# Optimization experiments

Measured on AMD Instinct MI355X. Metric: run time of the kernel, lower is better.

The kernel has to match this reference:

```python
import jax, jax.numpy as jnp
import numpy as np

B, N, C = 128, 36, 1024
K_NB = 16            # neighbors per node (top-k, includes loop)
KERNEL = 8           # number of Gaussian kernels
OUT = 1024           # out_dim; per-kernel out = OUT // KERNEL
PI = np.float32(np.pi)


def setup_inputs() -> dict:
    key = jax.random.key(0)
    ks = jax.random.split(key, 9)
    node_feats = jax.random.normal(ks[0], (B, N, C), dtype=jnp.float32)
    node_centre = jax.random.uniform(ks[1], (B, N, 2), dtype=jnp.float32)
    neighbor_idx = jax.random.randint(ks[2], (B * N, K_NB), 0, B * N, dtype=jnp.int32)
    graph_weights = jax.random.uniform(ks[3], (B * N * K_NB, 1), dtype=jnp.float32)
    # Gaussian kernel params (per reset_parameters)
    mean_rho = jax.random.uniform(ks[4], (1, KERNEL), dtype=jnp.float32)
    mean_theta = jax.random.uniform(ks[5], (1, KERNEL), minval=-PI, maxval=PI, dtype=jnp.float32)
    precision_rho = jax.random.uniform(ks[6], (1, KERNEL), minval=0.5, maxval=1.0, dtype=jnp.float32)
    precision_theta = jax.random.uniform(ks[7], (1, KERNEL), minval=0.5, maxval=1.0, dtype=jnp.float32)
    # per-kernel Linear(node_dim, out_dim//kernel, bias=False), stacked: [K, d_out_k, C]
    conv_w = jax.random.normal(ks[8], (KERNEL, OUT // KERNEL, C), dtype=jnp.float32) * (1.0 / np.sqrt(C))
    return {
        "node_feats": node_feats,
        "node_centre": node_centre,
        "neighbor_idx": neighbor_idx,
        "graph_weights": graph_weights,
        "mean_rho": mean_rho,
        "mean_theta": mean_theta,
        "precision_rho": precision_rho,
        "precision_theta": precision_theta,
        "conv_w": conv_w,
    }


def _forward(node_feats, node_centre, graph_weights,
             mean_rho, mean_theta, precision_rho, precision_theta,
             conv_w, neighbor_idx):
    b, n, c = node_feats.shape
    bn = b * n
    # pseudo polar coordinates per edge: centre_i - centre_j
    centre = node_centre.reshape(bn, 2)                       # [BN, 2]
    diff = centre[:, None, :] - centre[neighbor_idx]          # [BN, K_nb, 2]
    coord_x = diff[..., 0].reshape(-1)                        # [E]
    coord_y = diff[..., 1].reshape(-1)
    rho = jnp.sqrt(coord_x ** 2 + coord_y ** 2)
    theta = jnp.arctan2(coord_x, coord_y)
    # Gaussian mixture membership weights over KERNEL kernels
    w_rho = jnp.exp(-0.5 * (rho[:, None] - mean_rho) ** 2 / (1e-14 + precision_rho ** 2))
    first_angle = jnp.abs(theta[:, None] - mean_theta)
    second_angle = jnp.abs(2.0 * PI - first_angle)
    w_theta = jnp.exp(-0.5 * jnp.minimum(first_angle, second_angle) ** 2 / (1e-14 + precision_theta ** 2))
    weights = w_rho * w_theta                                  # [E, KERNEL]
    weights = jnp.where(jnp.isnan(weights), 0.0, weights)
    weights = weights / jnp.sum(weights, axis=1, keepdims=True)
    # combine with graph edge weights
    edge_w = graph_weights * weights                           # [E, KERNEL]
    edge_w = edge_w.reshape(bn, K_NB, KERNEL).transpose(0, 2, 1)  # [BN, K, K_nb]
    # gather neighbor features and weighted aggregate (bmm)
    nbr = node_feats.reshape(bn, c)[neighbor_idx]              # [BN, K_nb, C]
    agg = jnp.einsum('ekn,enc->ekc', edge_w, nbr)              # [BN, KERNEL, C]
    agg = agg.reshape(b, n, KERNEL, c)
    # per-kernel linear then concat over kernel dim
    out = jnp.einsum('bnkc,kdc->bnkd', agg, conv_w)            # [B, N, KERNEL, OUT//KERNEL]
    out = out.reshape(b, n, -1)                                # [B, N, OUT]
    return jax.nn.relu(out)


def reference(node_feats, node_centre, neighbor_idx, graph_weights,
              mean_rho, mean_theta, precision_rho, precision_theta, conv_w):
    return _forward(node_feats, node_centre, graph_weights,
                    mean_rho, mean_theta, precision_rho, precision_theta,
                    conv_w, neighbor_idx)
```

## Files before the change

kernel.cpp:

```cpp
#include <hip/hip_runtime.h>
#include <hip/hip_bf16.h>
#include <stdint.h>

#define B_DIM   128
#define N_DIM   36
#define C_DIM   1024
#define KNB     16
#define NKER    8
#define OUTD    1024
#define BN_NODES (B_DIM * N_DIM)
#define E_EDGES  (BN_NODES * KNB)
#define PI_F 3.14159265358979323846f

#define TM 64
#define TN 128
#define BK 64
#define KIT (C_DIM / BK)
#define CLP 136
#define A_OFF(p) ((p) * TM * BK)
#define B_OFF(p) (2 * TM * BK + (p) * TN * BK)

typedef __attribute__((ext_vector_type(8))) short bf16x8;
typedef __attribute__((ext_vector_type(4))) float floatx4;

struct alignas(8) U16x4 { unsigned short x, y, z, w; };

__device__ __forceinline__ unsigned short f2bf(float f) {
  union { float f; uint32_t u; } v; v.f = f;
  uint32_t u = v.u;
  return (unsigned short)((u + 0x7fffu + ((u >> 16) & 1u)) >> 16);
}
__device__ __forceinline__ float bf2f_lo(uint32_t pair) {
  union { uint32_t u; float f; } v; v.u = pair << 16;
  return v.f;
}
__device__ __forceinline__ float bf2f_hi(uint32_t pair) {
  union { uint32_t u; float f; } v; v.u = pair & 0xffff0000u;
  return v.f;
}

__device__ __forceinline__ void gload16(const void* g, void* l) {
  __builtin_amdgcn_global_load_lds((__attribute__((address_space(1))) void*)(g),
                                   (__attribute__((address_space(3))) void*)(l),
                                   16, 0, 0);
}

__global__ __launch_bounds__(256)
void cast_ew_kernel(const float* __restrict__ feats,
                    const float* __restrict__ cw,
                    const float* __restrict__ centre,
                    const int*   __restrict__ nbr,
                    const float* __restrict__ gw,
                    const float* __restrict__ mrho,
                    const float* __restrict__ mth,
                    const float* __restrict__ prho,
                    const float* __restrict__ pth,
                    unsigned short* __restrict__ fb,
                    unsigned short* __restrict__ wb,
                    float* __restrict__ ewg)
{
  const int NF4 = (BN_NODES * C_DIM) / 4;
  const int NW4 = (C_DIM * OUTD) / 4;
  int tid = blockIdx.x * 256 + threadIdx.x;
  if (tid < NF4) {
    float4 v = ((const float4*)feats)[tid];
    U16x4 o = { f2bf(v.x), f2bf(v.y), f2bf(v.z), f2bf(v.w) };
    ((U16x4*)fb)[tid] = o;
  } else {
    int t = tid - NF4;
    if (t < NW4) {
      float4 v = ((const float4*)cw)[t];
      U16x4 o = { f2bf(v.x), f2bf(v.y), f2bf(v.z), f2bf(v.w) };
      ((U16x4*)wb)[t] = o;
    } else {
      int e = t - NW4;
      if (e < E_EDGES) {
        int n = e >> 4;
        int m = nbr[e];
        float cx = centre[2 * n]     - centre[2 * m];
        float cy = centre[2 * n + 1] - centre[2 * m + 1];
        float rho   = sqrtf(cx * cx + cy * cy);
        float theta = atan2f(cx, cy);
        float wk[NKER];
        float s = 0.f;
#pragma unroll
        for (int k = 0; k < NKER; ++k) {
          float dr = rho - mrho[k];
          float pr = prho[k];
          float w_r = expf(-0.5f * dr * dr / (1e-14f + pr * pr));
          float fa = fabsf(theta - mth[k]);
          float sa = fabsf(2.0f * PI_F - fa);
          float mm = fminf(fa, sa);
          float pt = pth[k];
          float w_t = expf(-0.5f * mm * mm / (1e-14f + pt * pt));
          float ww = w_r * w_t;
          wk[k] = (ww != ww) ? 0.f : ww;
          s += wk[k];
        }
        float scale = gw[e] / s;
        int j = e & 15;
#pragma unroll
        for (int k = 0; k < NKER; ++k)
          ewg[(size_t)n * (NKER * KNB) + k * KNB + j] = wk[k] * scale;
      }
    }
  }
}

__global__ __launch_bounds__(256)
void gemm_bt(const unsigned short* __restrict__ A,
             const unsigned short* __restrict__ Bt,
             unsigned short* __restrict__ D)
{
  __shared__ unsigned short smem[2 * TM * BK + 2 * TN * BK];

  const int tid  = threadIdx.x;
  const int lane = tid & 63;
  const int wave = tid >> 6;
  const int wm   = wave >> 1;
  const int wn   = wave & 1;
  const int row0 = blockIdx.x * TM;
  const int col0 = blockIdx.y * TN;

  const int q  = lane >> 4;
  const int lr = lane & 15;

  floatx4 acc[2][4] = {};

  int offA[2], offB[4];
#pragma unroll
  for (int i = 0; i < 2; ++i) {
    int c = tid + 256 * i, row = c >> 3, qc = c & 7;
    offA[i] = (row0 + row) * C_DIM + (qc ^ (row & 7)) * 8;
  }
#pragma unroll
  for (int i = 0; i < 4; ++i) {
    int c = tid + 256 * i, row = c >> 3, qc = c & 7;
    offB[i] = (col0 + row) * C_DIM + (qc ^ (row & 7)) * 8;
  }

#define DMA(T, P) do {                                                       \
    _Pragma("unroll") for (int i = 0; i < 2; ++i)                            \
      gload16(A + offA[i] + (T) * BK,                                        \
              &smem[A_OFF(P) + (tid + 256 * i) * 8]);                        \
    _Pragma("unroll") for (int i = 0; i < 4; ++i)                            \
      gload16(Bt + offB[i] + (T) * BK,                                       \
              &smem[B_OFF(P) + (tid + 256 * i) * 8]);                        \
  } while (0)

  DMA(0, 0);

  for (int t = 0; t < KIT; ++t) {
    const int p = t & 1;
    __syncthreads();
    if (t + 1 < KIT) DMA(t + 1, 1 - p);

    const int aBase = A_OFF(p);
    const int bBase = B_OFF(p);
#pragma unroll
    for (int kc = 0; kc < 2; ++kc) {
      const int sc = ((kc * 4 + q) ^ (lr & 7)) * 8;
      bf16x8 af[2], bfr[4];
#pragma unroll
      for (int i = 0; i < 2; ++i)
        af[i]  = *(const bf16x8*)&smem[aBase + (wm * 32 + i * 16 + lr) * BK + sc];
#pragma unroll
      for (int j = 0; j < 4; ++j)
        bfr[j] = *(const bf16x8*)&smem[bBase + (wn * 64 + j * 16 + lr) * BK + sc];
#pragma unroll
      for (int i = 0; i < 2; ++i)
#pragma unroll
        for (int j = 0; j < 4; ++j)
          acc[i][j] = __builtin_amdgcn_mfma_f32_16x16x32_bf16(
              af[i], bfr[j], acc[i][j], 0, 0, 0);
    }
  }
#undef DMA

  __syncthreads();
#pragma unroll
  for (int i = 0; i < 2; ++i)
#pragma unroll
    for (int j = 0; j < 4; ++j)
#pragma unroll
      for (int r = 0; r < 4; ++r)
        smem[(wm * 32 + i * 16 + q * 4 + r) * CLP + wn * 64 + j * 16 + lr] =
            f2bf(acc[i][j][r]);
  __syncthreads();
#pragma unroll
  for (int i = 0; i < 4; ++i) {
    int c = tid + 256 * i;
    int row = c >> 4, qc = c & 15;
    *(uint4*)&D[(size_t)(row0 + row) * OUTD + col0 + qc * 8] =
        *(const uint4*)&smem[row * CLP + qc * 8];
  }
}

__global__ __launch_bounds__(256)
void agg_gather(const unsigned short* __restrict__ proj,
                const int*   __restrict__ nbr,
                const float* __restrict__ ewg,
                float* __restrict__ out)
{
  __shared__ int   idx[8][KNB];
  __shared__ float ewl[8][2][KNB];

  const int bid = blockIdx.x;
  const int x   = bid & 7;
  const int s   = x >> 1;
  const int g   = ((bid >> 3) << 1) | (x & 1);
  const int n0  = g * 8;
  const int t   = threadIdx.x;

  if (t < 128)
    idx[t >> 4][t & 15] = nbr[(n0 + (t >> 4)) * KNB + (t & 15)];
  {
    int a = t >> 5, r = t & 31;
    ewl[a][r >> 4][r & 15] = ewg[(size_t)(n0 + a) * (NKER * KNB) + s * 32 + r];
  }
  __syncthreads();

  const int a   = t >> 5;
  const int cu  = t & 31;
  const int kk  = cu >> 4;
  const int n   = n0 + a;
  const int ch0 = s * 256 + cu * 8;

  float acc[8] = {0.f, 0.f, 0.f, 0.f, 0.f, 0.f, 0.f, 0.f};
#pragma unroll
  for (int j = 0; j < KNB; ++j) {
    float wv = ewl[a][kk][j];
    uint4 v = *(const uint4*)&proj[(size_t)idx[a][j] * OUTD + ch0];
    acc[0] += wv * bf2f_lo(v.x);  acc[1] += wv * bf2f_hi(v.x);
    acc[2] += wv * bf2f_lo(v.y);  acc[3] += wv * bf2f_hi(v.y);
    acc[4] += wv * bf2f_lo(v.z);  acc[5] += wv * bf2f_hi(v.z);
    acc[6] += wv * bf2f_lo(v.w);  acc[7] += wv * bf2f_hi(v.w);
  }
  float4 r0, r1;
  r0.x = fmaxf(acc[0], 0.f); r0.y = fmaxf(acc[1], 0.f);
  r0.z = fmaxf(acc[2], 0.f); r0.w = fmaxf(acc[3], 0.f);
  r1.x = fmaxf(acc[4], 0.f); r1.y = fmaxf(acc[5], 0.f);
  r1.z = fmaxf(acc[6], 0.f); r1.w = fmaxf(acc[7], 0.f);
  float* o = out + (size_t)n * OUTD + ch0;
  *(float4*)(o)     = r0;
  *(float4*)(o + 4) = r1;
}

extern "C" void kernel_launch(void* const* d_in, const int* in_sizes, int n_in,
                              void* d_out, int out_size, void* d_ws, size_t ws_size,
                              hipStream_t stream)
{
  const float* feats  = (const float*)d_in[0];
  const float* centre = (const float*)d_in[1];
  const int*   nbr    = (const int*)  d_in[2];
  const float* gw     = (const float*)d_in[3];
  const float* mrho   = (const float*)d_in[4];
  const float* mth    = (const float*)d_in[5];
  const float* prho   = (const float*)d_in[6];
  const float* pth    = (const float*)d_in[7];
  const float* cw     = (const float*)d_in[8];
  float* out = (float*)d_out;

  char* ws = (char*)d_ws;
  unsigned short* fb   = (unsigned short*)(ws);
  unsigned short* wb   = (unsigned short*)(ws + 9437184);
  unsigned short* proj = (unsigned short*)(ws + 11534336);
  float*          ewg  = (float*)         (ws + 20971520);

  const int NF4 = (BN_NODES * C_DIM) / 4;
  const int NW4 = (C_DIM * OUTD) / 4;
  const int EWB = (E_EDGES + 255) / 256;
  cast_ew_kernel<<<dim3((NF4 + NW4) / 256 + EWB), dim3(256), 0, stream>>>(
      feats, cw, centre, nbr, gw, mrho, mth, prho, pth, fb, wb, ewg);
  gemm_bt<<<dim3(BN_NODES / TM, OUTD / TN), dim3(256), 0, stream>>>(fb, wb, proj);
  agg_gather<<<dim3(BN_NODES / 2), dim3(256), 0, stream>>>(proj, nbr, ewg, out);
}
```

Baseline: 122.3 us.

## Fuse fp32-to-bf16 feature cast into GEMM A-tile loads

Removes the separate pass that converts node features to bf16 in workspace. The GEMM now reads fp32 features straight from global memory into registers, converts them, and writes bf16 into shared memory. This saves one full read-write round trip of the feature matrix. The row tile shrinks from 64 to 48 and the wave layout changes to 1x4, so the grid divides evenly over 4608 rows. In exchange the A operand now uses register-staged loads instead of direct global-to-LDS DMA, and each block does less work.

```diff
diff --git a/kernel.cpp b/kernel.cpp
--- a/kernel.cpp
+++ b/kernel.cpp
@@ -12,7 +12,7 @@
 #define E_EDGES  (BN_NODES * KNB)
 #define PI_F 3.14159265358979323846f
 
-#define TM 64
+#define TM 48
 #define TN 128
 #define BK 64
 #define KIT (C_DIM / BK)
@@ -23,7 +23,8 @@
 typedef __attribute__((ext_vector_type(8))) short bf16x8;
 typedef __attribute__((ext_vector_type(4))) float floatx4;
 
-struct alignas(8) U16x4 { unsigned short x, y, z, w; };
+struct alignas(8)  U16x4 { unsigned short x, y, z, w; };
+struct alignas(16) U16x8 { unsigned short s[8]; };
 
 __device__ __forceinline__ unsigned short f2bf(float f) {
   union { float f; uint32_t u; } v; v.f = f;
@@ -46,149 +47,161 @@
 }
 
 __global__ __launch_bounds__(256)
-void cast_ew_kernel(const float* __restrict__ feats,
-                    const float* __restrict__ cw,
-                    const float* __restrict__ centre,
-                    const int*   __restrict__ nbr,
-                    const float* __restrict__ gw,
-                    const float* __restrict__ mrho,
-                    const float* __restrict__ mth,
-                    const float* __restrict__ prho,
-                    const float* __restrict__ pth,
-                    unsigned short* __restrict__ fb,
-                    unsigned short* __restrict__ wb,
-                    float* __restrict__ ewg)
-{
-  const int NF4 = (BN_NODES * C_DIM) / 4;
+void castw_ew_kernel(const float* __restrict__ cw,
+                     const float* __restrict__ centre,
+                     const int*   __restrict__ nbr,
+                     const float* __restrict__ gw,
+                     const float* __restrict__ mrho,
+                     const float* __restrict__ mth,
+                     const float* __restrict__ prho,
+                     const float* __restrict__ pth,
+                     unsigned short* __restrict__ wb,
+                     float* __restrict__ ewg)
+{
   const int NW4 = (C_DIM * OUTD) / 4;
   int tid = blockIdx.x * 256 + threadIdx.x;
-  if (tid < NF4) {
-    float4 v = ((const float4*)feats)[tid];
+  if (tid < NW4) {
+    float4 v = ((const float4*)cw)[tid];
     U16x4 o = { f2bf(v.x), f2bf(v.y), f2bf(v.z), f2bf(v.w) };
-    ((U16x4*)fb)[tid] = o;
+    ((U16x4*)wb)[tid] = o;
   } else {
-    int t = tid - NF4;
-    if (t < NW4) {
-      float4 v = ((const float4*)cw)[t];
-      U16x4 o = { f2bf(v.x), f2bf(v.y), f2bf(v.z), f2bf(v.w) };
-      ((U16x4*)wb)[t] = o;
-    } else {
-      int e = t - NW4;
-      if (e < E_EDGES) {
-        int n = e >> 4;
-        int m = nbr[e];
-        float cx = centre[2 * n]     - centre[2 * m];
-        float cy = centre[2 * n + 1] - centre[2 * m + 1];
-        float rho   = sqrtf(cx * cx + cy * cy);
-        float theta = atan2f(cx, cy);
-        float wk[NKER];
-        float s = 0.f;
-#pragma unroll
-        for (int k = 0; k < NKER; ++k) {
-          float dr = rho - mrho[k];
-          float pr = prho[k];
-          float w_r = expf(-0.5f * dr * dr / (1e-14f + pr * pr));
-          float fa = fabsf(theta - mth[k]);
-          float sa = fabsf(2.0f * PI_F - fa);
-          float mm = fminf(fa, sa);
-          float pt = pth[k];
-          float w_t = expf(-0.5f * mm * mm / (1e-14f + pt * pt));
-          float ww = w_r * w_t;
-          wk[k] = (ww != ww) ? 0.f : ww;
-          s += wk[k];
-        }
-        float scale = gw[e] / s;
-        int j = e & 15;
-#pragma unroll
-        for (int k = 0; k < NKER; ++k)
-          ewg[(size_t)n * (NKER * KNB) + k * KNB + j] = wk[k] * scale;
+    int e = tid - NW4;
+    if (e < E_EDGES) {
+      int n = e >> 4;
+      int m = nbr[e];
+      float cx = centre[2 * n]     - centre[2 * m];
+      float cy = centre[2 * n + 1] - centre[2 * m + 1];
+      float rho   = sqrtf(cx * cx + cy * cy);
+      float theta = atan2f(cx, cy);
+      float wk[NKER];
+      float s = 0.f;
+#pragma unroll
+      for (int k = 0; k < NKER; ++k) {
+        float dr = rho - mrho[k];
+        float pr = prho[k];
+        float w_r = expf(-0.5f * dr * dr / (1e-14f + pr * pr));
+        float fa = fabsf(theta - mth[k]);
+        float sa = fabsf(2.0f * PI_F - fa);
+        float mm = fminf(fa, sa);
+        float pt = pth[k];
+        float w_t = expf(-0.5f * mm * mm / (1e-14f + pt * pt));
+        float ww = w_r * w_t;
+        wk[k] = (ww != ww) ? 0.f : ww;
+        s += wk[k];
       }
+      float scale = gw[e] / s;
+      int j = e & 15;
+#pragma unroll
+      for (int k = 0; k < NKER; ++k)
+        ewg[(size_t)n * (NKER * KNB) + k * KNB + j] = wk[k] * scale;
     }
   }
 }
 
 __global__ __launch_bounds__(256)
-void gemm_bt(const unsigned short* __restrict__ A,
-             const unsigned short* __restrict__ Bt,
-             unsigned short* __restrict__ D)
+void gemm_fused(const float* __restrict__ A,
+                const unsigned short* __restrict__ Bt,
+                unsigned short* __restrict__ D)
 {
   __shared__ unsigned short smem[2 * TM * BK + 2 * TN * BK];
 
   const int tid  = threadIdx.x;
   const int lane = tid & 63;
-  const int wave = tid >> 6;
-  const int wm   = wave >> 1;
-  const int wn   = wave & 1;
+  const int wv   = tid >> 6;
   const int row0 = blockIdx.x * TM;
   const int col0 = blockIdx.y * TN;
 
   const int q  = lane >> 4;
   const int lr = lane & 15;
 
-  floatx4 acc[2][4] = {};
-
-  int offA[2], offB[4];
-#pragma unroll
-  for (int i = 0; i < 2; ++i) {
-    int c = tid + 256 * i, row = c >> 3, qc = c & 7;
-    offA[i] = (row0 + row) * C_DIM + (qc ^ (row & 7)) * 8;
-  }
+  floatx4 acc[3][2] = {};
+
+  int offB[4];
 #pragma unroll
   for (int i = 0; i < 4; ++i) {
     int c = tid + 256 * i, row = c >> 3, qc = c & 7;
     offB[i] = (col0 + row) * C_DIM + (qc ^ (row & 7)) * 8;
   }
 
-#define DMA(T, P) do {                                                       \
-    _Pragma("unroll") for (int i = 0; i < 2; ++i)                            \
-      gload16(A + offA[i] + (T) * BK,                                        \
-              &smem[A_OFF(P) + (tid + 256 * i) * 8]);                        \
+  const int r0A = tid >> 3;
+  const int gA0 = (row0 + r0A) * C_DIM + (tid & 7) * 8;
+  const int r2A = 32 + (tid >> 4);
+  const int gA2 = (row0 + r2A) * C_DIM + (tid & 15) * 4;
+  const int wA0 = r0A * BK + (((tid & 7) ^ (r0A & 7)) * 8);
+  const int wA2 = r2A * BK + ((((tid >> 1) & 7) ^ (r2A & 7)) * 8) + (tid & 1) * 4;
+
+  float4 a0, a1, a2;
+
+#define LOADA(T) do {                                                        \
+    a0 = *(const float4*)&A[gA0 + (T) * BK];                                 \
+    a1 = *(const float4*)&A[gA0 + 4 + (T) * BK];                             \
+    a2 = *(const float4*)&A[gA2 + (T) * BK];                                 \
+  } while (0)
+
+#define WRITEA(P) do {                                                       \
+    U16x8 w8;                                                                \
+    w8.s[0] = f2bf(a0.x); w8.s[1] = f2bf(a0.y);                              \
+    w8.s[2] = f2bf(a0.z); w8.s[3] = f2bf(a0.w);                              \
+    w8.s[4] = f2bf(a1.x); w8.s[5] = f2bf(a1.y);                              \
+    w8.s[6] = f2bf(a1.z); w8.s[7] = f2bf(a1.w);                              \
+    *(U16x8*)&smem[A_OFF(P) + wA0] = w8;                                     \
+    U16x4 w4 = { f2bf(a2.x), f2bf(a2.y), f2bf(a2.z), f2bf(a2.w) };           \
+    *(U16x4*)&smem[A_OFF(P) + wA2] = w4;                                     \
+  } while (0)
+
+#define DMAB(T, P) do {                                                      \
     _Pragma("unroll") for (int i = 0; i < 4; ++i)                            \
       gload16(Bt + offB[i] + (T) * BK,                                       \
               &smem[B_OFF(P) + (tid + 256 * i) * 8]);                        \
   } while (0)
 
-  DMA(0, 0);
+  LOADA(0);
+  DMAB(0, 0);
+  WRITEA(0);
+  __syncthreads();
 
   for (int t = 0; t < KIT; ++t) {
     const int p = t & 1;
-    __syncthreads();
-    if (t + 1 < KIT) DMA(t + 1, 1 - p);
+    if (t + 1 < KIT) { DMAB(t + 1, 1 - p); LOADA(t + 1); }
 
     const int aBase = A_OFF(p);
     const int bBase = B_OFF(p);
 #pragma unroll
     for (int kc = 0; kc < 2; ++kc) {
-      const int sc = ((kc * 4 + q) ^ (lr & 7)) * 8;
-      bf16x8 af[2], bfr[4];
-#pragma unroll
-      for (int i = 0; i < 2; ++i)
-        af[i]  = *(const bf16x8*)&smem[aBase + (wm * 32 + i * 16 + lr) * BK + sc];
-#pragma unroll
-      for (int j = 0; j < 4; ++j)
-        bfr[j] = *(const bf16x8*)&smem[bBase + (wn * 64 + j * 16 + lr) * BK + sc];
-#pragma unroll
-      for (int i = 0; i < 2; ++i)
-#pragma unroll
-        for (int j = 0; j < 4; ++j)
+      const int sc = ((kc * 4 + q) ^ (lr & 15 & 7)) * 8;
+      bf16x8 af[3], bfr[2];
+#pragma unroll
+      for (int i = 0; i < 3; ++i)
+        af[i]  = *(const bf16x8*)&smem[aBase + (i * 16 + lr) * BK + sc];
+#pragma unroll
+      for (int j = 0; j < 2; ++j)
+        bfr[j] = *(const bf16x8*)&smem[bBase + (wv * 32 + j * 16 + lr) * BK + sc];
+#pragma unroll
+      for (int i = 0; i < 3; ++i)
+#pragma unroll
+        for (int j = 0; j < 2; ++j)
           acc[i][j] = __builtin_amdgcn_mfma_f32_16x16x32_bf16(
               af[i], bfr[j], acc[i][j], 0, 0, 0);
     }
-  }
-#undef DMA
-
-  __syncthreads();
-#pragma unroll
-  for (int i = 0; i < 2; ++i)
-#pragma unroll
-    for (int j = 0; j < 4; ++j)
+
+    if (t + 1 < KIT) WRITEA(1 - p);
+    __syncthreads();
+  }
+#undef LOADA
+#undef WRITEA
+#undef DMAB
+
+#pragma unroll
+  for (int i = 0; i < 3; ++i)
+#pragma unroll
+    for (int j = 0; j < 2; ++j)
 #pragma unroll
       for (int r = 0; r < 4; ++r)
-        smem[(wm * 32 + i * 16 + q * 4 + r) * CLP + wn * 64 + j * 16 + lr] =
+        smem[(i * 16 + q * 4 + r) * CLP + wv * 32 + j * 16 + lr] =
             f2bf(acc[i][j][r]);
   __syncthreads();
 #pragma unroll
-  for (int i = 0; i < 4; ++i) {
+  for (int i = 0; i < 3; ++i) {
     int c = tid + 256 * i;
     int row = c >> 4, qc = c & 15;
     *(uint4*)&D[(size_t)(row0 + row) * OUTD + col0 + qc * 8] =
@@ -229,12 +242,12 @@
   float acc[8] = {0.f, 0.f, 0.f, 0.f, 0.f, 0.f, 0.f, 0.f};
 #pragma unroll
   for (int j = 0; j < KNB; ++j) {
-    float wv = ewl[a][kk][j];
+    float wvv = ewl[a][kk][j];
     uint4 v = *(const uint4*)&proj[(size_t)idx[a][j] * OUTD + ch0];
-    acc[0] += wv * bf2f_lo(v.x);  acc[1] += wv * bf2f_hi(v.x);
-    acc[2] += wv * bf2f_lo(v.y);  acc[3] += wv * bf2f_hi(v.y);
-    acc[4] += wv * bf2f_lo(v.z);  acc[5] += wv * bf2f_hi(v.z);
-    acc[6] += wv * bf2f_lo(v.w);  acc[7] += wv * bf2f_hi(v.w);
+    acc[0] += wvv * bf2f_lo(v.x);  acc[1] += wvv * bf2f_hi(v.x);
+    acc[2] += wvv * bf2f_lo(v.y);  acc[3] += wvv * bf2f_hi(v.y);
+    acc[4] += wvv * bf2f_lo(v.z);  acc[5] += wvv * bf2f_hi(v.z);
+    acc[6] += wvv * bf2f_lo(v.w);  acc[7] += wvv * bf2f_hi(v.w);
   }
   float4 r0, r1;
   r0.x = fmaxf(acc[0], 0.f); r0.y = fmaxf(acc[1], 0.f);
@@ -262,16 +275,15 @@
   float* out = (float*)d_out;
 
   char* ws = (char*)d_ws;
-  unsigned short* fb   = (unsigned short*)(ws);
-  unsigned short* wb   = (unsigned short*)(ws + 9437184);
-  unsigned short* proj = (unsigned short*)(ws + 11534336);
-  float*          ewg  = (float*)         (ws + 20971520);
-
-  const int NF4 = (BN_NODES * C_DIM) / 4;
+  unsigned short* wb   = (unsigned short*)(ws);
+  unsigned short* proj = (unsigned short*)(ws + 2097152);
+  float*          ewg  = (float*)         (ws + 11534336);
+
   const int NW4 = (C_DIM * OUTD) / 4;
   const int EWB = (E_EDGES + 255) / 256;
-  cast_ew_kernel<<<dim3((NF4 + NW4) / 256 + EWB), dim3(256), 0, stream>>>(
-      feats, cw, centre, nbr, gw, mrho, mth, prho, pth, fb, wb, ewg);
-  gemm_bt<<<dim3(BN_NODES / TM, OUTD / TN), dim3(256), 0, stream>>>(fb, wb, proj);
+  castw_ew_kernel<<<dim3(NW4 / 256 + EWB), dim3(256), 0, stream>>>(
+      cw, centre, nbr, gw, mrho, mth, prho, pth, wb, ewg);
+  gemm_fused<<<dim3(BN_NODES / TM, OUTD / TN), dim3(256), 0, stream>>>(
+      feats, wb, proj);
   agg_gather<<<dim3(BN_NODES / 2), dim3(256), 0, stream>>>(proj, nbr, ewg, out);
 }
```

Result: no change. 121.6 us (-0.5%).
